# Kernel optimization log

Hardware: AMD Instinct MI355X
Metric: run time of the kernel (lower is better)

## Reference

```python
import jax, jax.numpy as jnp
import numpy as np

N_ATOMS = 100000
N_EDGES = 1600000
N_GRAPHS = 64
N_BASIS = 128
N_FILTERS = 128
N_RBF = 32
N_INTER = 6
CUTOFF = 10.0
LOG2 = float(np.log(2.0))


def ssp(x):
    # shifted softplus
    return jax.nn.softplus(x) - LOG2


def setup_inputs() -> dict:
    key = jax.random.key(0)
    ks = jax.random.split(key, 24)
    s = 0.05
    inp = {
        "z": jax.random.randint(ks[0], (N_ATOMS,), 0, 100),
        "z_res": jax.random.randint(ks[1], (N_ATOMS,), 0, 100),
        "pos": jax.random.normal(ks[2], (N_ATOMS, 3), jnp.float32) * 5.0,
        "idx_i": jax.random.randint(ks[3], (N_EDGES,), 0, N_ATOMS),
        "idx_j": jax.random.randint(ks[4], (N_EDGES,), 0, N_ATOMS),
        "edge_attr": jax.random.randint(ks[5], (N_EDGES,), 0, 4),
        "batch": jnp.sort(jax.random.randint(ks[6], (N_ATOMS,), 0, N_GRAPHS)),
        "ele_emb": jax.random.normal(ks[7], (100, N_BASIS), jnp.float32) * s,
        "res_emb": jax.random.normal(ks[8], (100, N_BASIS), jnp.float32) * s,
        "edge_emb": jax.random.normal(ks[9], (4, N_RBF), jnp.float32) * s,
        "in2f_W": jax.random.normal(ks[10], (N_INTER, N_BASIS, N_FILTERS), jnp.float32) * s,
        "filt_W1": jax.random.normal(ks[11], (N_INTER, N_RBF, N_FILTERS), jnp.float32) * s,
        "filt_b1": jnp.zeros((N_INTER, N_FILTERS), jnp.float32),
        "filt_W2": jax.random.normal(ks[12], (N_INTER, N_FILTERS, N_FILTERS), jnp.float32) * s,
        "filt_b2": jnp.zeros((N_INTER, N_FILTERS), jnp.float32),
        "f2out_W1": jax.random.normal(ks[13], (N_INTER, N_FILTERS, N_BASIS), jnp.float32) * s,
        "f2out_b1": jnp.zeros((N_INTER, N_BASIS), jnp.float32),
        "f2out_W2": jax.random.normal(ks[14], (N_INTER, N_BASIS, N_BASIS), jnp.float32) * s,
        "f2out_b2": jnp.zeros((N_INTER, N_BASIS), jnp.float32),
        "head_W1": jax.random.normal(ks[15], (N_BASIS, N_BASIS), jnp.float32) * s,
        "head_b1": jnp.zeros((N_BASIS,), jnp.float32),
        "head_W2": jax.random.normal(ks[16], (N_BASIS, 1), jnp.float32) * s,
    }
    return inp


def _forward(z, z_res, pos, idx_i, idx_j, edge_attr, batch,
             ele_emb, res_emb, edge_emb,
             in2f_W, filt_W1, filt_b1, filt_W2, filt_b2,
             f2out_W1, f2out_b1, f2out_W2, f2out_b2,
             head_W1, head_b1, head_W2):
    # distances per edge
    r_ij = pos[idx_i] - pos[idx_j]                       # [E,3]
    d_ij = jnp.linalg.norm(r_ij, axis=1)                 # [E]

    # Gaussian RBF expansion: offsets linspace(0, cutoff, n_rbf)
    offsets = jnp.linspace(0.0, CUTOFF, N_RBF)
    width = offsets[1] - offsets[0]
    coeff = -0.5 / (width * width)
    f_ij = jnp.exp(coeff * (d_ij[:, None] - offsets[None, :]) ** 2)  # [E,R]
    f_ij = f_ij + edge_emb[edge_attr]

    # cosine cutoff
    rcut_ij = 0.5 * (jnp.cos(d_ij * jnp.pi / CUTOFF) + 1.0) * (d_ij < CUTOFF)

    # atom embeddings
    x = ele_emb[z] + res_emb[z_res]                      # [N,B]

    for i in range(N_INTER):
        xf = x @ in2f_W[i]                               # [N,F]
        Wij = ssp(f_ij @ filt_W1[i] + filt_b1[i]) @ filt_W2[i] + filt_b2[i]
        Wij = Wij * rcut_ij[:, None]                     # [E,F]
        x_ij = xf[idx_j] * Wij                           # gather + multiply
        agg = jax.ops.segment_sum(x_ij, idx_i, num_segments=N_ATOMS)  # scatter_add
        v = ssp(agg @ f2out_W1[i] + f2out_b1[i]) @ f2out_W2[i] + f2out_b2[i]
        x = x + v

    # L2 normalize then head
    h = x / jnp.maximum(jnp.linalg.norm(x, axis=-1, keepdims=True), 1e-12)
    h = jax.nn.silu(h) @ head_W1 + head_b1
    h = jax.nn.silu(h) @ head_W2                         # [N,1]
    new_y = jax.ops.segment_sum(h, batch, num_segments=N_GRAPHS)  # [G,1]
    return new_y.squeeze(-1)


def reference(z, z_res, pos, idx_i, idx_j, edge_attr, batch,
              ele_emb, res_emb, edge_emb,
              in2f_W, filt_W1, filt_b1, filt_W2, filt_b2,
              f2out_W1, f2out_b1, f2out_W2, f2out_b2,
              head_W1, head_b1, head_W2):
    return _forward(z, z_res, pos, idx_i, idx_j, edge_attr, batch,
                    ele_emb, res_emb, edge_emb,
                    in2f_W, filt_W1, filt_b1, filt_W2, filt_b2,
                    f2out_W1, f2out_b1, f2out_W2, f2out_b2,
                    head_W1, head_b1, head_W2)
```

## Files before the change

### kernel.cpp

```cpp
#include <hip/hip_runtime.h>
#include <hip/hip_bf16.h>
#include <math.h>

#define NB 128
#define NR 32
#define EPAD 40
#define HPAD 136
#define SCB 256


static constexpr float CUTOFF_F    = 10.0f;
static constexpr float RBF_STEP    = 10.0f / 31.0f;
static constexpr float RBF_COEFF   = -4.805f;
static constexpr float LOG2_F      = 0.69314718055994531f;
static constexpr float PI_OVER_CUT = 0.314159265358979f;

typedef __attribute__((ext_vector_type(8))) short bf16x8;
typedef __attribute__((ext_vector_type(2))) short bf16x2;
typedef __attribute__((ext_vector_type(4))) float f32x4;

__device__ __forceinline__ short f2bs(float x) {
    __hip_bfloat16 h = __float2bfloat16(x);
    return *reinterpret_cast<short*>(&h);
}
__device__ __forceinline__ float bs2f(unsigned short u) {
    unsigned int v = ((unsigned int)u) << 16;
    return __uint_as_float(v);
}
__device__ __forceinline__ float ssp_f(float v) {
    return fmaxf(v, 0.0f) + __logf(1.0f + __expf(-fabsf(v))) - LOG2_F;
}
__device__ __forceinline__ float silu_f(float v) {
    return v / (1.0f + __expf(-v));
}

__device__ __forceinline__ void atomic_pk_add_bf16(short* addr, float lo, float hi) {
#if __has_builtin(__builtin_amdgcn_global_atomic_fadd_v2bf16)
    typedef bf16x2 __attribute__((address_space(1))) *gptr;
    bf16x2 v;
    v[0] = f2bs(lo);
    v[1] = f2bs(hi);
    __builtin_amdgcn_global_atomic_fadd_v2bf16((gptr)(unsigned long long)addr, v);
#else
    unsigned int* w = (unsigned int*)addr;
    unsigned int old = *w, assumed;
    do {
        assumed = old;
        float fl = bs2f((unsigned short)(assumed & 0xffff)) + lo;
        float fh = bs2f((unsigned short)(assumed >> 16)) + hi;
        unsigned int nv = ((unsigned int)(unsigned short)f2bs(fh) << 16) |
                          (unsigned short)f2bs(fl);
        old = atomicCAS(w, assumed, nv);
    } while (old != assumed);
#endif
}

__device__ __forceinline__ void flush_pk(short* aggrow, const float* accum, int col) {
    bool even = ((col & 1) == 0);
#pragma unroll
    for (int q = 0; q < 4; q++) {
        float a = accum[2 * q], b = accum[2 * q + 1];
        float pa = __shfl_xor(a, 1);
        float pb = __shfl_xor(b, 1);
        int nbase = even ? (2 * q) * 16 + col : (2 * q + 1) * 16 + (col - 1);
        float lo = even ? a : pb;
        float hi = even ? pa : b;
        atomic_pk_add_bf16(aggrow + nbase, lo, hi);
    }
}

__global__ void transpose_cvt(const float* __restrict__ src, short* __restrict__ dst,
                              int R, int C, int total) {
    int t = blockIdx.x * blockDim.x + threadIdx.x;
    if (t >= total) return;
    int rc = R * C;
    int b = t / rc;
    int rem = t - b * rc;
    int c = rem / R;
    int r = rem - c * R;
    dst[t] = f2bs(src[(size_t)b * rc + (size_t)r * C + c]);
}

__global__ void edge_prep4(const float* __restrict__ pos,
                           const int* __restrict__ idx_i,
                           const int* __restrict__ idx_j,
                           float* __restrict__ d_ij,
                           int* __restrict__ hist,
                           int E) {
    int b0 = blockIdx.x * 1024 + threadIdx.x;
    int ia[4], ib[4];
    bool val[4];
#pragma unroll
    for (int k = 0; k < 4; k++) {
        int e = b0 + k * 256;
        val[k] = (e < E);
        ia[k] = val[k] ? idx_i[e] : 0;
        ib[k] = val[k] ? idx_j[e] : 0;
    }
    float ax[4], ay[4], az[4], bx[4], by[4], bz[4];
#pragma unroll
    for (int k = 0; k < 4; k++) {
        const float* pa = pos + ia[k] * 3;
        ax[k] = pa[0]; ay[k] = pa[1]; az[k] = pa[2];
    }
#pragma unroll
    for (int k = 0; k < 4; k++) {
        const float* pb = pos + ib[k] * 3;
        bx[k] = pb[0]; by[k] = pb[1]; bz[k] = pb[2];
    }
#pragma unroll
    for (int k = 0; k < 4; k++) {
        if (!val[k]) continue;
        float dx = ax[k] - bx[k], dy = ay[k] - by[k], dz = az[k] - bz[k];
        float d = sqrtf(dx * dx + dy * dy + dz * dz);
        d_ij[b0 + k * 256] = d;
        if (d < CUTOFF_F) atomicAdd(&hist[ia[k]], 1);
    }
}

__global__ __launch_bounds__(256) void scan_reduce(const int* __restrict__ hist,
                                                   int* __restrict__ partial, int N) {
    __shared__ int red[256];
    int b = blockIdx.x;
    int chunk = (N + SCB - 1) / SCB;
    int lo = b * chunk;
    int hi = min(lo + chunk, N);
    int s = 0;
    for (int i = lo + threadIdx.x; i < hi; i += 256) s += hist[i];
    red[threadIdx.x] = s;
    __syncthreads();
    for (int d = 128; d > 0; d >>= 1) {
        if (threadIdx.x < d) red[threadIdx.x] += red[threadIdx.x + d];
        __syncthreads();
    }
    if (threadIdx.x == 0) partial[b] = red[0];
}

__global__ __launch_bounds__(256) void scan_partials(int* __restrict__ partial) {
    __shared__ int sm[SCB];
    int t = threadIdx.x;
    sm[t] = partial[t];
    __syncthreads();
    for (int d = 1; d < SCB; d <<= 1) {
        int v = (t >= d) ? sm[t - d] : 0;
        __syncthreads();
        sm[t] += v;
        __syncthreads();
    }
    partial[t] = (t == 0) ? 0 : sm[t - 1];
}

__global__ __launch_bounds__(256) void scan_expand(const int* __restrict__ hist,
                                                   const int* __restrict__ partial,
                                                   int* __restrict__ cursor, int N) {
    __shared__ int tsum[256];
    int b = blockIdx.x;
    int chunk = (N + SCB - 1) / SCB;
    int lo = b * chunk;
    int hi = min(lo + chunk, N);
    int sub = (chunk + 255) / 256;
    int tlo = lo + threadIdx.x * sub;
    int thi = min(tlo + sub, hi);
    int s = 0;
    for (int i = tlo; i < thi; i++) s += hist[i];
    int t = threadIdx.x;
    tsum[t] = s;
    __syncthreads();
    for (int d = 1; d < 256; d <<= 1) {
        int v = (t >= d) ? tsum[t - d] : 0;
        __syncthreads();
        tsum[t] += v;
        __syncthreads();
    }
    int run = partial[b] + ((t == 0) ? 0 : tsum[t - 1]);
    for (int i = tlo; i < thi; i++) {
        cursor[i] = run;
        run += hist[i];
    }
}

__global__ void scatter_sorted4(const float* __restrict__ d_ij,
                                const int* __restrict__ idx_i,
                                const int* __restrict__ idx_j,
                                const int* __restrict__ edge_attr,
                                int* __restrict__ cursor,
                                float4* __restrict__ edata,
                                int* __restrict__ sIarr, int E) {
    int b0 = blockIdx.x * 1024 + threadIdx.x;
    float d[4]; int ii[4], jj[4], at[4]; bool act[4];
#pragma unroll
    for (int k = 0; k < 4; k++) {
        int e = b0 + k * 256;
        bool v = (e < E);
        d[k] = v ? d_ij[e] : 1e9f;
        act[k] = (d[k] < CUTOFF_F);
        ii[k] = act[k] ? idx_i[e] : 0;
        jj[k] = act[k] ? idx_j[e] : 0;
        at[k] = act[k] ? edge_attr[e] : 0;
    }
    int p[4];
#pragma unroll
    for (int k = 0; k < 4; k++)
        if (act[k]) p[k] = atomicAdd(&cursor[ii[k]], 1);
#pragma unroll
    for (int k = 0; k < 4; k++) {
        if (!act[k]) continue;
        float4 v;
        v.x = d[k];
        v.y = 0.5f * (__cosf(d[k] * PI_OVER_CUT) + 1.0f);
        v.z = __int_as_float(jj[k]);
        v.w = __int_as_float(at[k]);
        edata[p[k]] = v;
        sIarr[p[k]] = ii[k];
    }
}

__global__ void atom_embed(const int* __restrict__ z,
                           const int* __restrict__ z_res,
                           const float* __restrict__ ele_emb,
                           const float* __restrict__ res_emb,
                           float* __restrict__ x, int N) {
    int t = blockIdx.x * blockDim.x + threadIdx.x;
    if (t >= N * NB) return;
    int n = t >> 7, c = t & 127;
    x[t] = ele_emb[z[n] * NB + c] + res_emb[z_res[n] * NB + c];
}

__global__ __launch_bounds__(256, 4) void node_in2f_mfma(
    const float* __restrict__ x, const short* __restrict__ WT,
    short* __restrict__ xf, int N) {
    __shared__ __align__(16) short XA[64 * HPAD];
    int a0 = blockIdx.x * 64;
    int t = threadIdx.x;
#pragma unroll
    for (int c = 0; c < 4; c++) {
        int chunk = t + c * 256;
        int row = chunk >> 4;
        int col = (chunk & 15) * 8;
        short v[8];
        if (a0 + row < N) {
            const float* src = x + (size_t)(a0 + row) * NB + col;
            float4 f0 = *(const float4*)src;
            float4 f1 = *(const float4*)(src + 4);
            v[0] = f2bs(f0.x); v[1] = f2bs(f0.y); v[2] = f2bs(f0.z); v[3] = f2bs(f0.w);
            v[4] = f2bs(f1.x); v[5] = f2bs(f1.y); v[6] = f2bs(f1.z); v[7] = f2bs(f1.w);
        } else {
#pragma unroll
            for (int j = 0; j < 8; j++) v[j] = 0;
        }
        *(bf16x8*)&XA[row * HPAD + col] = *(bf16x8*)v;
    }
    __syncthreads();

    int wid = t >> 6, lane = t & 63;
    int quad = lane >> 4, col = lane & 15;
    int mrow = wid * 16 + col;

    f32x4 acc[8] = {};
#pragma unroll
    for (int kt = 0; kt < 4; kt++) {
        bf16x8 a = *(bf16x8*)&XA[mrow * HPAD + kt * 32 + quad * 8];
#pragma unroll
        for (int nt = 0; nt < 8; nt++) {
            bf16x8 b = *(const bf16x8*)&WT[(nt * 16 + col) * NB + kt * 32 + quad * 8];
            acc[nt] = __builtin_amdgcn_mfma_f32_16x16x32_bf16(a, b, acc[nt], 0, 0, 0);
        }
    }
#pragma unroll
    for (int nt = 0; nt < 8; nt++) {
        int cst = col * 8 + nt;
#pragma unroll
        for (int r = 0; r < 4; r++) {
            int m = wid * 16 + quad * 4 + r;
            if (a0 + m < N) xf[(size_t)(a0 + m) * NB + cst] = f2bs(acc[nt][r]);
        }
    }
}

__global__ __launch_bounds__(256, 4) void node_fused_mfma(
    short* __restrict__ agg,
    const short* __restrict__ W1T, const float* __restrict__ b1,
    const short* __restrict__ W2T, const float* __restrict__ b2,
    const short* __restrict__ WnT,
    float* __restrict__ x, short* __restrict__ xf, int N) {
    __shared__ __align__(16) short XA[64 * HPAD];
    __shared__ __align__(16) short H[64 * HPAD];
    int a0 = blockIdx.x * 64;
    int t = threadIdx.x;
#pragma unroll
    for (int c = 0; c < 4; c++) {
        int chunk = t + c * 256;
        int row = chunk >> 4;
        int col = (chunk & 15) * 8;
        bf16x8 v = {0, 0, 0, 0, 0, 0, 0, 0};
        if (a0 + row < N) {
            short* src = agg + (size_t)(a0 + row) * NB + col;
            v = *(const bf16x8*)src;
            *(bf16x8*)src = (bf16x8){0, 0, 0, 0, 0, 0, 0, 0};
        }
        *(bf16x8*)&XA[row * HPAD + col] = v;
    }
    __syncthreads();

    int wid = t >> 6, lane = t & 63;
    int quad = lane >> 4, col = lane & 15;
    int mrow = wid * 16 + col;

    {
        f32x4 acc[8] = {};
#pragma unroll
        for (int kt = 0; kt < 4; kt++) {
            bf16x8 a = *(bf16x8*)&XA[mrow * HPAD + kt * 32 + quad * 8];
#pragma unroll
            for (int nt = 0; nt < 8; nt++) {
                bf16x8 b = *(const bf16x8*)&W1T[(nt * 16 + col) * NB + kt * 32 + quad * 8];
                acc[nt] = __builtin_amdgcn_mfma_f32_16x16x32_bf16(a, b, acc[nt], 0, 0, 0);
            }
        }
#pragma unroll
        for (int nt = 0; nt < 8; nt++) {
            int n = nt * 16 + col;
            float bias = b1[n];
#pragma unroll
            for (int r = 0; r < 4; r++) {
                int m = wid * 16 + quad * 4 + r;
                H[m * HPAD + n] = f2bs(ssp_f(acc[nt][r] + bias));
            }
        }
    }
    __syncthreads();

    {
        f32x4 acc[8] = {};
#pragma unroll
        for (int kt = 0; kt < 4; kt++) {
            bf16x8 a = *(bf16x8*)&H[mrow * HPAD + kt * 32 + quad * 8];
#pragma unroll
            for (int nt = 0; nt < 8; nt++) {
                bf16x8 b = *(const bf16x8*)&W2T[(nt * 16 + col) * NB + kt * 32 + quad * 8];
                acc[nt] = __builtin_amdgcn_mfma_f32_16x16x32_bf16(a, b, acc[nt], 0, 0, 0);
            }
        }
#pragma unroll
        for (int nt = 0; nt < 8; nt++) {
            int n = nt * 16 + col;
            float bias = b2[n];
#pragma unroll
            for (int r = 0; r < 4; r++) {
                int m = wid * 16 + quad * 4 + r;
                float xn = 0.0f;
                if (a0 + m < N) {
                    size_t o = (size_t)(a0 + m) * NB + n;
                    xn = x[o] + acc[nt][r] + bias;
                    x[o] = xn;
                }
                XA[m * HPAD + n] = f2bs(xn);
            }
        }
    }
    __syncthreads();

    {
        f32x4 acc[8] = {};
#pragma unroll
        for (int kt = 0; kt < 4; kt++) {
            bf16x8 a = *(bf16x8*)&XA[mrow * HPAD + kt * 32 + quad * 8];
#pragma unroll
            for (int nt = 0; nt < 8; nt++) {
                bf16x8 b = *(const bf16x8*)&WnT[(nt * 16 + col) * NB + kt * 32 + quad * 8];
                acc[nt] = __builtin_amdgcn_mfma_f32_16x16x32_bf16(a, b, acc[nt], 0, 0, 0);
            }
        }
#pragma unroll
        for (int nt = 0; nt < 8; nt++) {
            int cst = col * 8 + nt;
#pragma unroll
            for (int r = 0; r < 4; r++) {
                int m = wid * 16 + quad * 4 + r;
                if (a0 + m < N) xf[(size_t)(a0 + m) * NB + cst] = f2bs(acc[nt][r]);
            }
        }
    }
}

__global__ __launch_bounds__(256, 4) void node_out_head_mfma(
    const short* __restrict__ agg,
    const short* __restrict__ W1T, const float* __restrict__ b1,
    const short* __restrict__ W2T, const float* __restrict__ b2,
    const float* __restrict__ x, const int* __restrict__ batch,
    const short* __restrict__ hW1T, const float* __restrict__ hb1,
    const float* __restrict__ hW2,
    float* __restrict__ out, int N) {
    __shared__ __align__(16) short XA[64 * HPAD];
    __shared__ __align__(16) short H[64 * HPAD];
    __shared__ int sbat[64];
    __shared__ float rowval[64];
    int a0 = blockIdx.x * 64;
    int t = threadIdx.x;

    if (t < 64) sbat[t] = (a0 + t < N) ? batch[a0 + t] : -1;
#pragma unroll
    for (int c = 0; c < 4; c++) {
        int chunk = t + c * 256;
        int row = chunk >> 4;
        int col = (chunk & 15) * 8;
        bf16x8 v = {0, 0, 0, 0, 0, 0, 0, 0};
        if (a0 + row < N) v = *(const bf16x8*)&agg[(size_t)(a0 + row) * NB + col];
        *(bf16x8*)&XA[row * HPAD + col] = v;
    }
    __syncthreads();

    int wid = t >> 6, lane = t & 63;
    int quad = lane >> 4, col = lane & 15;
    int mrow = wid * 16 + col;

    {
        f32x4 acc[8] = {};
#pragma unroll
        for (int kt = 0; kt < 4; kt++) {
            bf16x8 a = *(bf16x8*)&XA[mrow * HPAD + kt * 32 + quad * 8];
#pragma unroll
            for (int nt = 0; nt < 8; nt++) {
                bf16x8 b = *(const bf16x8*)&W1T[(nt * 16 + col) * NB + kt * 32 + quad * 8];
                acc[nt] = __builtin_amdgcn_mfma_f32_16x16x32_bf16(a, b, acc[nt], 0, 0, 0);
            }
        }
#pragma unroll
        for (int nt = 0; nt < 8; nt++) {
            int n = nt * 16 + col;
            float bias = b1[n];
#pragma unroll
            for (int r = 0; r < 4; r++) {
                int m = wid * 16 + quad * 4 + r;
                H[m * HPAD + n] = f2bs(ssp_f(acc[nt][r] + bias));
            }
        }
    }
    __syncthreads();

    float xnv[8][4];
    float ssq[4] = {0.f, 0.f, 0.f, 0.f};
    {
        f32x4 acc[8] = {};
#pragma unroll
        for (int kt = 0; kt < 4; kt++) {
            bf16x8 a = *(bf16x8*)&H[mrow * HPAD + kt * 32 + quad * 8];
#pragma unroll
            for (int nt = 0; nt < 8; nt++) {
                bf16x8 b = *(const bf16x8*)&W2T[(nt * 16 + col) * NB + kt * 32 + quad * 8];
                acc[nt] = __builtin_amdgcn_mfma_f32_16x16x32_bf16(a, b, acc[nt], 0, 0, 0);
            }
        }
#pragma unroll
        for (int nt = 0; nt < 8; nt++) {
            int n = nt * 16 + col;
            float bias = b2[n];
#pragma unroll
            for (int r = 0; r < 4; r++) {
                int m = wid * 16 + quad * 4 + r;
                float xn = 0.0f;
                if (a0 + m < N) xn = x[(size_t)(a0 + m) * NB + n] + acc[nt][r] + bias;
                xnv[nt][r] = xn;
                ssq[r] += xn * xn;
            }
        }
    }
#pragma unroll
    for (int r = 0; r < 4; r++) {
#pragma unroll
        for (int m = 1; m < 16; m <<= 1) ssq[r] += __shfl_xor(ssq[r], m);
    }
    float inv[4];
#pragma unroll
    for (int r = 0; r < 4; r++) inv[r] = 1.0f / fmaxf(sqrtf(ssq[r]), 1e-12f);
    __syncthreads();
#pragma unroll
    for (int nt = 0; nt < 8; nt++) {
        int n = nt * 16 + col;
#pragma unroll
        for (int r = 0; r < 4; r++) {
            int m = wid * 16 + quad * 4 + r;
            XA[m * HPAD + n] = f2bs(silu_f(xnv[nt][r] * inv[r]));
        }
    }
    __syncthreads();

    f32x4 acc[8] = {};
#pragma unroll
    for (int kt = 0; kt < 4; kt++) {
        bf16x8 a = *(bf16x8*)&XA[mrow * HPAD + kt * 32 + quad * 8];
#pragma unroll
        for (int nt = 0; nt < 8; nt++) {
            bf16x8 b = *(const bf16x8*)&hW1T[(nt * 16 + col) * NB + kt * 32 + quad * 8];
            acc[nt] = __builtin_amdgcn_mfma_f32_16x16x32_bf16(a, b, acc[nt], 0, 0, 0);
        }
    }
    float partial[4] = {0.f, 0.f, 0.f, 0.f};
#pragma unroll
    for (int nt = 0; nt < 8; nt++) {
        int n = nt * 16 + col;
        float bias = hb1[n];
        float w2 = hW2[n];
#pragma unroll
        for (int r = 0; r < 4; r++) partial[r] += silu_f(acc[nt][r] + bias) * w2;
    }
#pragma unroll
    for (int r = 0; r < 4; r++) {
#pragma unroll
        for (int d = 1; d < 16; d <<= 1) partial[r] += __shfl_xor(partial[r], d);
    }
    if (col == 0) {
#pragma unroll
        for (int r = 0; r < 4; r++) rowval[wid * 16 + quad * 4 + r] = partial[r];
    }
    __syncthreads();

    if (t < 64) {
        int b = sbat[t];
        bool headf = (b >= 0) && (t == 0 || sbat[t - 1] != b);
        if (headf) {
            float s = 0.0f;
            int rr = t;
            while (rr < 64 && sbat[rr] == b) { s += rowval[rr]; rr++; }
            atomicAdd(&out[b], s);
        }
    }
}

__global__ __launch_bounds__(256, 3) void edge_fused_mfma(
    const float4* __restrict__ edata, const int* __restrict__ sIarr,
    const int* __restrict__ rowend, int natoms,
    const float* __restrict__ edge_emb,
    const short* __restrict__ W1T, const float* __restrict__ b1,
    const short* __restrict__ W2T, const float* __restrict__ b2,
    const short* __restrict__ xf, short* __restrict__ agg) {
    __shared__ __align__(16) short fA[128 * EPAD];
    __shared__ __align__(16) short H[128 * HPAD];

    int t = threadIdx.x;
    int wid = t >> 6, lane = t & 63;
    int quad = lane >> 4, col = lane & 15;
    int base = blockIdx.x * 128;
    int wbase = base + wid * 32;
    int el32 = lane & 31;

    float4 ed = edata[wbase + el32];
    int sIv0 = sIarr[wbase + el32];
    int cnt = rowend[natoms - 1];
    if (base >= cnt) return;

    bool act = (wbase + el32) < cnt;
    float dv  = act ? ed.x : 1e9f;
    float rcv = act ? ed.y : 0.0f;
    int   jjv = act ? __float_as_int(ed.z) : 0;
    int   atv = act ? __float_as_int(ed.w) : 0;
    int   iiv = act ? sIv0 : 0;

    {
        int elA = lane >> 1;
        int r0 = (lane & 1) * 16;
        float d  = __shfl(dv, elA);
        int   at = __shfl(atv, elA);
        const float* em = edge_emb + at * NR + r0;
        short v[16];
#pragma unroll
        for (int j = 0; j < 16; j++) {
            float off = (float)(r0 + j) * RBF_STEP;
            float dd = d - off;
            v[j] = f2bs(__expf(RBF_COEFF * dd * dd) + em[j]);
        }
        short* dst = &fA[(wid * 32 + elA) * EPAD + r0];
        *(bf16x8*)dst = *(bf16x8*)v;
        *(bf16x8*)(dst + 8) = *(bf16x8*)(v + 8);
    }

    bf16x8 xv[2][4];
    const unsigned short* xg = (const unsigned short*)xf;
#pragma unroll
    for (int s = 0; s < 2; s++) {
#pragma unroll
        for (int r = 0; r < 4; r++) {
            int jj = __shfl(jjv, s * 16 + quad * 4 + r);
            xv[s][r] = *(const bf16x8*)&xg[(size_t)jj * NB + col * 8];
        }
    }

    asm volatile("s_waitcnt lgkmcnt(0)" ::: "memory");
    __builtin_amdgcn_sched_barrier(0);

    {
        bf16x8 b1f[8];
#pragma unroll
        for (int nt = 0; nt < 8; nt++)
            b1f[nt] = *(const bf16x8*)&W1T[(nt * 16 + col) * NR + quad * 8];
#pragma unroll
        for (int s = 0; s < 2; s++) {
            bf16x8 a1 = *(bf16x8*)&fA[(wid * 32 + s * 16 + col) * EPAD + quad * 8];
            f32x4 acc[8];
#pragma unroll
            for (int nt = 0; nt < 8; nt++)
                acc[nt] = __builtin_amdgcn_mfma_f32_16x16x32_bf16(a1, b1f[nt], (f32x4){0.f, 0.f, 0.f, 0.f}, 0, 0, 0);
#pragma unroll
            for (int nt = 0; nt < 8; nt++) {
                int n = nt * 16 + col;
                float bias = b1[n];
#pragma unroll
                for (int r = 0; r < 4; r++) {
                    int m = wid * 32 + s * 16 + quad * 4 + r;
                    H[m * HPAD + n] = f2bs(ssp_f(acc[nt][r] + bias));
                }
            }
        }
    }

    asm volatile("s_waitcnt lgkmcnt(0)" ::: "memory");
    __builtin_amdgcn_sched_barrier(0);

    f32x4 acc2[2][8] = {};
#pragma unroll
    for (int kt = 0; kt < 4; kt++) {
        bf16x8 b2f[8];
#pragma unroll
        for (int nt = 0; nt < 8; nt++)
            b2f[nt] = *(const bf16x8*)&W2T[(nt * 16 + col) * NB + kt * 32 + quad * 8];
#pragma unroll
        for (int s = 0; s < 2; s++) {
            bf16x8 a = *(bf16x8*)&H[(wid * 32 + s * 16 + col) * HPAD + kt * 32 + quad * 8];
#pragma unroll
            for (int nt = 0; nt < 8; nt++)
                acc2[s][nt] = __builtin_amdgcn_mfma_f32_16x16x32_bf16(a, b2f[nt], acc2[s][nt], 0, 0, 0);
        }
    }

    float b2v[8];
#pragma unroll
    for (int nt = 0; nt < 8; nt++) b2v[nt] = b2[nt * 16 + col];

#pragma unroll
    for (int s = 0; s < 2; s++) {
        int e0l = s * 16 + quad * 4;
        int cur = __shfl(iiv, e0l);
        float accum[8] = {0.f, 0.f, 0.f, 0.f, 0.f, 0.f, 0.f, 0.f};
#pragma unroll
        for (int r = 0; r < 4; r++) {
            int ii = __shfl(iiv, e0l + r);
            float rc = __shfl(rcv, e0l + r);
            if (ii != cur) {
                flush_pk(agg + (size_t)cur * NB, accum, col);
#pragma unroll
                for (int nt = 0; nt < 8; nt++) accum[nt] = 0.f;
                cur = ii;
            }
#pragma unroll
            for (int nt = 0; nt < 8; nt++) {
                float w = (acc2[s][nt][r] + b2v[nt]) * rc;
                accum[nt] = fmaf(w, bs2f((unsigned short)xv[s][r][nt]), accum[nt]);
            }
        }
        flush_pk(agg + (size_t)cur * NB, accum, col);
    }
}

extern "C" void kernel_launch(void* const* d_in, const int* in_sizes, int n_in,
                              void* d_out, int out_size, void* d_ws, size_t ws_size,
                              hipStream_t stream) {
    const int*   z        = (const int*)d_in[0];
    const int*   z_res    = (const int*)d_in[1];
    const float* pos      = (const float*)d_in[2];
    const int*   idx_i    = (const int*)d_in[3];
    const int*   idx_j    = (const int*)d_in[4];
    const int*   edge_attr= (const int*)d_in[5];
    const int*   batch    = (const int*)d_in[6];
    const float* ele_emb  = (const float*)d_in[7];
    const float* res_emb  = (const float*)d_in[8];
    const float* edge_emb = (const float*)d_in[9];
    const float* in2f_W   = (const float*)d_in[10];
    const float* filt_W1  = (const float*)d_in[11];
    const float* filt_b1  = (const float*)d_in[12];
    const float* filt_W2  = (const float*)d_in[13];
    const float* filt_b2  = (const float*)d_in[14];
    const float* f2out_W1 = (const float*)d_in[15];
    const float* f2out_b1 = (const float*)d_in[16];
    const float* f2out_W2 = (const float*)d_in[17];
    const float* f2out_b2 = (const float*)d_in[18];
    const float* head_W1  = (const float*)d_in[19];
    const float* head_b1  = (const float*)d_in[20];
    const float* head_W2  = (const float*)d_in[21];

    const int N = in_sizes[0];
    const int E = in_sizes[3];

    char* p = (char*)d_ws;
    size_t off = 0;
    auto carve = [&](size_t bytes) -> void* {
        void* q = p + off;
        off = (off + bytes + 255) & ~(size_t)255;
        return q;
    };
    float*  d_d      = (float*)carve((size_t)E * 4);
    float4* edata    = (float4*)carve((size_t)E * 16);
    int*    sIarr    = (int*)carve((size_t)E * 4);
    int*    hist     = (int*)carve((size_t)N * 4);
    int*    cursor   = (int*)carve((size_t)N * 4);
    int*    partial  = (int*)carve((size_t)SCB * 4);
    float*  x_buf    = (float*)carve((size_t)N * NB * 4);
    short*  xf_buf   = (short*)carve((size_t)N * NB * 2);
    short*  agg      = (short*)carve((size_t)N * NB * 2);
    short*  in2f_WT  = (short*)carve((size_t)6 * NB * NB * 2);
    short*  fW1T     = (short*)carve((size_t)6 * NR * NB * 2);
    short*  fW2T     = (short*)carve((size_t)6 * NB * NB * 2);
    short*  oW1T     = (short*)carve((size_t)6 * NB * NB * 2);
    short*  oW2T     = (short*)carve((size_t)6 * NB * NB * 2);
    short*  hW1T     = (short*)carve((size_t)NB * NB * 2);
    (void)ws_size;

    {
        int tot = 6 * NB * NB;
        transpose_cvt<<<(tot + 255) / 256, 256, 0, stream>>>(in2f_W, in2f_WT, NB, NB, tot);
        transpose_cvt<<<(tot + 255) / 256, 256, 0, stream>>>(filt_W2, fW2T, NB, NB, tot);
        transpose_cvt<<<(tot + 255) / 256, 256, 0, stream>>>(f2out_W1, oW1T, NB, NB, tot);
        transpose_cvt<<<(tot + 255) / 256, 256, 0, stream>>>(f2out_W2, oW2T, NB, NB, tot);
        int tot1 = 6 * NR * NB;
        transpose_cvt<<<(tot1 + 255) / 256, 256, 0, stream>>>(filt_W1, fW1T, NR, NB, tot1);
        int tot2 = NB * NB;
        transpose_cvt<<<(tot2 + 255) / 256, 256, 0, stream>>>(head_W1, hW1T, NB, NB, tot2);
    }

    hipMemsetAsync(hist, 0, (size_t)N * 4, stream);
    int nblk_e4 = (E + 1023) / 1024;
    edge_prep4<<<nblk_e4, 256, 0, stream>>>(pos, idx_i, idx_j, d_d, hist, E);
    scan_reduce<<<SCB, 256, 0, stream>>>(hist, partial, N);
    scan_partials<<<1, SCB, 0, stream>>>(partial);
    scan_expand<<<SCB, 256, 0, stream>>>(hist, partial, cursor, N);
    scatter_sorted4<<<nblk_e4, 256, 0, stream>>>(d_d, idx_i, idx_j, edge_attr,
                                                 cursor, edata, sIarr, E);

    atom_embed<<<(N * NB + 255) / 256, 256, 0, stream>>>(z, z_res, ele_emb, res_emb, x_buf, N);

    int nblk_atom64 = (N + 63) / 64;
    int nblk_edge = (E + 127) / 128;

    node_in2f_mfma<<<nblk_atom64, 256, 0, stream>>>(x_buf, in2f_WT, xf_buf, N);
    hipMemsetAsync(d_out, 0, (size_t)out_size * sizeof(float), stream);
    hipMemsetAsync(agg, 0, (size_t)N * NB * 2, stream);
    for (int i = 0; i < 6; i++) {
        edge_fused_mfma<<<nblk_edge, 256, 0, stream>>>(
            edata, sIarr, cursor, N, edge_emb,
            fW1T + (size_t)i * NR * NB, filt_b1 + (size_t)i * NB,
            fW2T + (size_t)i * NB * NB, filt_b2 + (size_t)i * NB,
            xf_buf, agg);
        if (i < 5) {
            node_fused_mfma<<<nblk_atom64, 256, 0, stream>>>(
                agg, oW1T + (size_t)i * NB * NB, f2out_b1 + (size_t)i * NB,
                oW2T + (size_t)i * NB * NB, f2out_b2 + (size_t)i * NB,
                in2f_WT + (size_t)(i + 1) * NB * NB,
                x_buf, xf_buf, N);
        } else {
            node_out_head_mfma<<<nblk_atom64, 256, 0, stream>>>(
                agg, oW1T + (size_t)i * NB * NB, f2out_b1 + (size_t)i * NB,
                oW2T + (size_t)i * NB * NB, f2out_b2 + (size_t)i * NB,
                x_buf, batch, hW1T, head_b1, head_W2,
                (float*)d_out, N);
        }
    }
}
```

Measured before the change: 1.923 ms.

## Give each wave 32 rows in node kernel and drop block barriers

The node MLP kernel now runs with 128 threads (two waves) per 64-atom tile, each wave owning 32 rows instead of 16. Each wave loads its B weight fragments once per k-step and reuses them across two 16-row M subtiles, halving weight reads per row. Because each wave only reads the shared-memory rows it wrote itself, the block-wide __syncthreads are replaced by a local LDS waitcnt plus a scheduling barrier. In exchange, accumulator register use doubles and there are fewer waves per block to hide latency, with launch bounds relaxed to let the compiler use more registers.

```diff
diff --git a/kernel.cpp b/kernel.cpp
--- a/kernel.cpp
+++ b/kernel.cpp
@@ -277,7 +277,7 @@
     }
 }
 
-__global__ __launch_bounds__(256, 4) void node_fused_mfma(
+__global__ __launch_bounds__(128, 1) void node_fused_mfma(
     short* __restrict__ agg,
     const short* __restrict__ W1T, const float* __restrict__ b1,
     const short* __restrict__ W2T, const float* __restrict__ b2,
@@ -287,97 +287,123 @@
     __shared__ __align__(16) short H[64 * HPAD];
     int a0 = blockIdx.x * 64;
     int t = threadIdx.x;
-#pragma unroll
-    for (int c = 0; c < 4; c++) {
-        int chunk = t + c * 256;
-        int row = chunk >> 4;
-        int col = (chunk & 15) * 8;
+    int wid = t >> 6, lane = t & 63;
+    int quad = lane >> 4, col = lane & 15;
+
+#pragma unroll
+    for (int c = 0; c < 8; c++) {
+        int chunk = lane + c * 64;
+        int row = wid * 32 + (chunk >> 4);
+        int colb = (chunk & 15) * 8;
         bf16x8 v = {0, 0, 0, 0, 0, 0, 0, 0};
         if (a0 + row < N) {
-            short* src = agg + (size_t)(a0 + row) * NB + col;
+            short* src = agg + (size_t)(a0 + row) * NB + colb;
             v = *(const bf16x8*)src;
             *(bf16x8*)src = (bf16x8){0, 0, 0, 0, 0, 0, 0, 0};
         }
-        *(bf16x8*)&XA[row * HPAD + col] = v;
-    }
-    __syncthreads();
-
-    int wid = t >> 6, lane = t & 63;
-    int quad = lane >> 4, col = lane & 15;
-    int mrow = wid * 16 + col;
+        *(bf16x8*)&XA[row * HPAD + colb] = v;
+    }
+    asm volatile("s_waitcnt lgkmcnt(0)" ::: "memory");
+    __builtin_amdgcn_sched_barrier(0);
 
     {
-        f32x4 acc[8] = {};
+        f32x4 acc[2][8] = {};
 #pragma unroll
         for (int kt = 0; kt < 4; kt++) {
-            bf16x8 a = *(bf16x8*)&XA[mrow * HPAD + kt * 32 + quad * 8];
+            bf16x8 bf[8];
+#pragma unroll
+            for (int nt = 0; nt < 8; nt++)
+                bf[nt] = *(const bf16x8*)&W1T[(nt * 16 + col) * NB + kt * 32 + quad * 8];
+#pragma unroll
+            for (int s = 0; s < 2; s++) {
+                bf16x8 a = *(bf16x8*)&XA[(wid * 32 + s * 16 + col) * HPAD + kt * 32 + quad * 8];
+#pragma unroll
+                for (int nt = 0; nt < 8; nt++)
+                    acc[s][nt] = __builtin_amdgcn_mfma_f32_16x16x32_bf16(a, bf[nt], acc[s][nt], 0, 0, 0);
+            }
+        }
+#pragma unroll
+        for (int s = 0; s < 2; s++) {
 #pragma unroll
             for (int nt = 0; nt < 8; nt++) {
-                bf16x8 b = *(const bf16x8*)&W1T[(nt * 16 + col) * NB + kt * 32 + quad * 8];
-                acc[nt] = __builtin_amdgcn_mfma_f32_16x16x32_bf16(a, b, acc[nt], 0, 0, 0);
-            }
-        }
-#pragma unroll
-        for (int nt = 0; nt < 8; nt++) {
-            int n = nt * 16 + col;
-            float bias = b1[n];
-#pragma unroll
-            for (int r = 0; r < 4; r++) {
-                int m = wid * 16 + quad * 4 + r;
-                H[m * HPAD + n] = f2bs(ssp_f(acc[nt][r] + bias));
-            }
-        }
-    }
-    __syncthreads();
+                int n = nt * 16 + col;
+                float bias = b1[n];
+#pragma unroll
+                for (int r = 0; r < 4; r++) {
+                    int m = wid * 32 + s * 16 + quad * 4 + r;
+                    H[m * HPAD + n] = f2bs(ssp_f(acc[s][nt][r] + bias));
+                }
+            }
+        }
+    }
+    asm volatile("s_waitcnt lgkmcnt(0)" ::: "memory");
+    __builtin_amdgcn_sched_barrier(0);
 
     {
-        f32x4 acc[8] = {};
+        f32x4 acc[2][8] = {};
 #pragma unroll
         for (int kt = 0; kt < 4; kt++) {
-            bf16x8 a = *(bf16x8*)&H[mrow * HPAD + kt * 32 + quad * 8];
+            bf16x8 bf[8];
+#pragma unroll
+            for (int nt = 0; nt < 8; nt++)
+                bf[nt] = *(const bf16x8*)&W2T[(nt * 16 + col) * NB + kt * 32 + quad * 8];
+#pragma unroll
+            for (int s = 0; s < 2; s++) {
+                bf16x8 a = *(bf16x8*)&H[(wid * 32 + s * 16 + col) * HPAD + kt * 32 + quad * 8];
+#pragma unroll
+                for (int nt = 0; nt < 8; nt++)
+                    acc[s][nt] = __builtin_amdgcn_mfma_f32_16x16x32_bf16(a, bf[nt], acc[s][nt], 0, 0, 0);
+            }
+        }
+#pragma unroll
+        for (int s = 0; s < 2; s++) {
 #pragma unroll
             for (int nt = 0; nt < 8; nt++) {
-                bf16x8 b = *(const bf16x8*)&W2T[(nt * 16 + col) * NB + kt * 32 + quad * 8];
-                acc[nt] = __builtin_amdgcn_mfma_f32_16x16x32_bf16(a, b, acc[nt], 0, 0, 0);
-            }
-        }
-#pragma unroll
-        for (int nt = 0; nt < 8; nt++) {
-            int n = nt * 16 + col;
-            float bias = b2[n];
-#pragma unroll
-            for (int r = 0; r < 4; r++) {
-                int m = wid * 16 + quad * 4 + r;
-                float xn = 0.0f;
-                if (a0 + m < N) {
-                    size_t o = (size_t)(a0 + m) * NB + n;
-                    xn = x[o] + acc[nt][r] + bias;
-                    x[o] = xn;
+                int n = nt * 16 + col;
+                float bias = b2[n];
+#pragma unroll
+                for (int r = 0; r < 4; r++) {
+                    int m = wid * 32 + s * 16 + quad * 4 + r;
+                    float xn = 0.0f;
+                    if (a0 + m < N) {
+                        size_t o = (size_t)(a0 + m) * NB + n;
+                        xn = x[o] + acc[s][nt][r] + bias;
+                        x[o] = xn;
+                    }
+                    XA[m * HPAD + n] = f2bs(xn);
                 }
-                XA[m * HPAD + n] = f2bs(xn);
-            }
-        }
-    }
-    __syncthreads();
+            }
+        }
+    }
+    asm volatile("s_waitcnt lgkmcnt(0)" ::: "memory");
+    __builtin_amdgcn_sched_barrier(0);
 
     {
-        f32x4 acc[8] = {};
+        f32x4 acc[2][8] = {};
 #pragma unroll
         for (int kt = 0; kt < 4; kt++) {
-            bf16x8 a = *(bf16x8*)&XA[mrow * HPAD + kt * 32 + quad * 8];
+            bf16x8 bf[8];
+#pragma unroll
+            for (int nt = 0; nt < 8; nt++)
+                bf[nt] = *(const bf16x8*)&WnT[(nt * 16 + col) * NB + kt * 32 + quad * 8];
+#pragma unroll
+            for (int s = 0; s < 2; s++) {
+                bf16x8 a = *(bf16x8*)&XA[(wid * 32 + s * 16 + col) * HPAD + kt * 32 + quad * 8];
+#pragma unroll
+                for (int nt = 0; nt < 8; nt++)
+                    acc[s][nt] = __builtin_amdgcn_mfma_f32_16x16x32_bf16(a, bf[nt], acc[s][nt], 0, 0, 0);
+            }
+        }
+#pragma unroll
+        for (int s = 0; s < 2; s++) {
 #pragma unroll
             for (int nt = 0; nt < 8; nt++) {
-                bf16x8 b = *(const bf16x8*)&WnT[(nt * 16 + col) * NB + kt * 32 + quad * 8];
-                acc[nt] = __builtin_amdgcn_mfma_f32_16x16x32_bf16(a, b, acc[nt], 0, 0, 0);
-            }
-        }
-#pragma unroll
-        for (int nt = 0; nt < 8; nt++) {
-            int cst = col * 8 + nt;
-#pragma unroll
-            for (int r = 0; r < 4; r++) {
-                int m = wid * 16 + quad * 4 + r;
-                if (a0 + m < N) xf[(size_t)(a0 + m) * NB + cst] = f2bs(acc[nt][r]);
+                int cst = col * 8 + nt;
+#pragma unroll
+                for (int r = 0; r < 4; r++) {
+                    int m = wid * 32 + s * 16 + quad * 4 + r;
+                    if (a0 + m < N) xf[(size_t)(a0 + m) * NB + cst] = f2bs(acc[s][nt][r]);
+                }
             }
         }
     }
@@ -750,7 +776,7 @@
             fW2T + (size_t)i * NB * NB, filt_b2 + (size_t)i * NB,
             xf_buf, agg);
         if (i < 5) {
-            node_fused_mfma<<<nblk_atom64, 256, 0, stream>>>(
+            node_fused_mfma<<<nblk_atom64, 128, 0, stream>>>(
                 agg, oW1T + (size_t)i * NB * NB, f2out_b1 + (size_t)i * NB,
                 oW2T + (size_t)i * NB * NB, f2out_b2 + (size_t)i * NB,
                 in2f_WT + (size_t)(i + 1) * NB * NB,
```

Result: faster. 1.875 ms, median of 2 (-2.5%).
